# Performance work log

Hardware: AMD Instinct MI355X
Metric: run time of the kernel (lower is better)

## Reference

```python
import jax, jax.numpy as jnp
import numpy as np

# module hyperparameters (from init_kwargs)
K = 32          # out_channels / features per branch
THRESH = 20.0   # firing threshold
KWTA = 4        # winners per branch
RF = 512        # rf_size (number of branches)
L = 2048        # receptive-field length
T = 32          # timesteps (leading 'batch' dim in SpykeTorch)
C = 1           # in_channels


def setup_inputs() -> dict:
    key = jax.random.key(0)
    k1, k2, k3 = jax.random.split(key, 3)
    rec_field = jax.random.uniform(k1, (T, C, RF, L), dtype=jnp.float32)
    W = jax.random.normal(k2, (RF, K, C, L), dtype=jnp.float32)  # per-branch local-conv weights
    reward = jax.random.normal(k3, (1, 1, RF), dtype=jnp.float32)
    return {"rec_field": rec_field, "W": W, "reward": reward}


def _winner_mask(thr, spikes):
    """SpykeTorch sf.get_k_winners for a single branch with 1x1 spatial output.
    thr, spikes: (T, K) thresholded potentials and their sign (0/1).
    Returns a (K,) 0/1 mask over the kwta winning features.
    Score = earliest-spike-dominant total potential, exactly as in SpykeTorch:
      first  = T - sum_t spikes           (first spike time, clamped)
      values = thr[first, k]
      total  = sum_t (spikes*values + spikes * max(spikes*values)*T)
    With 1x1 spatial, inhibition_radius has no effect; picking then zeroing a
    feature == distinct top-k over features with a nonzero check.
    """
    first = jnp.clip((T - spikes.sum(0)).astype(jnp.int32), 0, T - 1)          # (K,)
    vals_at_first = jnp.take_along_axis(thr, first[None, :], axis=0)[0]        # (K,)
    trunc = spikes * vals_at_first[None, :]                                    # (T, K)
    v = trunc.max() * T
    total = (trunc + spikes * v).sum(0)                                        # (K,)
    top_vals, top_idx = jax.lax.top_k(total, KWTA)
    valid = (top_vals != 0).astype(thr.dtype)
    return jnp.zeros((K,), thr.dtype).at[top_idx].max(valid)


def reference(rec_field, W, reward):
    # per-branch local convolution: kernel covers the whole (1,L) input -> 1x1 output
    pot = jnp.einsum('tcrl,rkcl->rtk', rec_field, W)        # (RF, T, K)
    # sf.fire: keep potentials strictly above threshold (F.threshold semantics)
    thr = jnp.where(pot > THRESH, pot, jnp.zeros((), pot.dtype))
    spikes = jnp.sign(thr)
    # kWTA winner masks per branch (coefs), then masked sign
    mask = jax.vmap(_winner_mask)(thr, spikes)              # (RF, K)
    out = jnp.sign(thr * mask[:, None, :])                  # (RF, T, K)
    # torch: cat(dim=2) -> (T,K,RF,1) -> squeeze -> (T,K,RF) -> unsqueeze(1) -> (T,1,K,RF)
    return jnp.transpose(out, (1, 2, 0))[:, None, :, :]
```

## Files before the change

### kernel.cpp

```cpp
#include <hip/hip_runtime.h>
#include <cstdint>


typedef float vf4 __attribute__((ext_vector_type(4)));
typedef float vf2 __attribute__((ext_vector_type(2)));

#define RFN 512
#define TN  32
#define KN  32
#define LN  2048
#define CHUNK 128
#define NITER (LN / CHUNK)

__global__ __launch_bounds__(512, 4) void column1_fused(
    const float* __restrict__ rec,
    const float* __restrict__ wgt,
    float* __restrict__ out)
{
    __shared__ __align__(16) float lds[2 * 64 * CHUNK];
    __shared__ float thr_s[32 * 33];
    __shared__ float nspk_s[32], vals_s[32], cand_s[32], tot_s[32], mask_s[32];

    const int r    = blockIdx.x;
    const int tid  = threadIdx.x;
    const int lane = tid & 63;
    const int wv   = tid >> 6;
    const int tg   = lane >> 3;
    const int kg   = lane & 7;

    const int c4 = tid & 31;
    const int r0 = tid >> 5;
    const float* gsrc[4];
    int ldoff[4];
#pragma unroll
    for (int s = 0; s < 4; ++s) {
        const int row = r0 + 16 * s;
        const float* g;
        if (row < 32) g = rec + ((size_t)(row * RFN + r)) * LN + (c4 << 2);
        else          g = wgt + ((size_t)(r * KN + (row - 32))) * LN + (c4 << 2);
        gsrc[s]  = g;
        ldoff[s] = row * CHUNK + ((c4 ^ (row & 31)) << 2);
    }

    vf4 stage[4];
#pragma unroll
    for (int s = 0; s < 4; ++s)
        stage[s] = __builtin_nontemporal_load((const vf4*)gsrc[s]);

    float acc[4][4];
#pragma unroll
    for (int jt = 0; jt < 4; ++jt)
#pragma unroll
        for (int jk = 0; jk < 4; ++jk) acc[jt][jk] = 0.0f;

    for (int it = 0; it < NITER; ++it) {
        float* buf = lds + (it & 1) * (64 * CHUNK);
#pragma unroll
        for (int s = 0; s < 4; ++s) *(vf4*)(buf + ldoff[s]) = stage[s];
        __syncthreads();
        if (it + 1 < NITER) {
#pragma unroll
            for (int s = 0; s < 4; ++s) {
                gsrc[s] += CHUNK;
                stage[s] = __builtin_nontemporal_load((const vf4*)gsrc[s]);
            }
        }
        const float* rs  = buf;
        const float* wsh = buf + 32 * CHUNK;
#pragma unroll
        for (int q = 0; q < 4; ++q) {
            const int qg = (wv << 2) + q;
            vf4 a[4], b[4];
#pragma unroll
            for (int j = 0; j < 4; ++j) {
                const int row = tg + 8 * j;
                a[j] = *(const vf4*)(rs + row * CHUNK + ((qg ^ (row & 31)) << 2));
            }
#pragma unroll
            for (int j = 0; j < 4; ++j) {
                const int row = kg + 8 * j;
                b[j] = *(const vf4*)(wsh + row * CHUNK + ((qg ^ (row & 31)) << 2));
            }
#pragma unroll
            for (int jt = 0; jt < 4; ++jt)
#pragma unroll
                for (int jk = 0; jk < 4; ++jk) {
                    float v0 = fmaf(a[jt].x, b[jk].x, acc[jt][jk]);
                    v0 = fmaf(a[jt].y, b[jk].y, v0);
                    v0 = fmaf(a[jt].z, b[jk].z, v0);
                    acc[jt][jk] = fmaf(a[jt].w, b[jk].w, v0);
                }
        }
    }

    __syncthreads();

    float* red = lds;
#pragma unroll
    for (int jt = 0; jt < 4; ++jt)
#pragma unroll
        for (int jk = 0; jk < 4; ++jk)
            red[(wv << 10) + (tg + 8 * jt) * 32 + (kg + 8 * jk)] = acc[jt][jk];
    __syncthreads();

    const int o2 = tid << 1;
    float pv0 = 0.0f, pv1 = 0.0f;
#pragma unroll
    for (int s = 0; s < 8; ++s) {
        vf2 p = *(const vf2*)(red + (s << 10) + o2);
        pv0 += p.x; pv1 += p.y;
    }
    {
        const float th0 = (pv0 > 20.0f) ? pv0 : 0.0f;
        const float th1 = (pv1 > 20.0f) ? pv1 : 0.0f;
        thr_s[(o2 >> 5) * 33 + (o2 & 31)]             = th0;
        thr_s[((o2 + 1) >> 5) * 33 + ((o2 + 1) & 31)] = th1;
    }
    __syncthreads();

    if (tid < 32) {
        const int k = tid;
        int ns = 0;
        for (int t = 0; t < 32; ++t) ns += (thr_s[t * 33 + k] > 0.0f) ? 1 : 0;
        int first = 32 - ns; if (first > 31) first = 31;
        const float vf = thr_s[first * 33 + k];
        nspk_s[k] = (float)ns;
        vals_s[k] = vf;
        cand_s[k] = (ns > 0) ? vf : 0.0f;
        mask_s[k] = 0.0f;
    }
    __syncthreads();

    if (tid == 0) {
        float vm = 0.0f;
        for (int k = 0; k < 32; ++k) vm = fmaxf(vm, cand_s[k]);
        const float v = vm * 32.0f;
        for (int k = 0; k < 32; ++k) tot_s[k] = nspk_s[k] * (vals_s[k] + v);
        for (int sel = 0; sel < 4; ++sel) {
            int best = 0; float bv = -1.0f;
            for (int k = 0; k < 32; ++k) {
                const float tv = tot_s[k];
                if (tv > bv) { bv = tv; best = k; }
            }
            if (bv > 0.0f) mask_s[best] = 1.0f;
            tot_s[best] = -1.0f;
        }
    }
    __syncthreads();

#pragma unroll
    for (int e = 0; e < 2; ++e) {
        const int oo = o2 + e;
        const int t = oo >> 5, k = oo & 31;
        const float v = (thr_s[t * 33 + k] > 0.0f && mask_s[k] > 0.0f) ? 1.0f : 0.0f;
        __builtin_nontemporal_store(v, out + (size_t)t * (KN * RFN) + k * RFN + r);
    }
}

extern "C" void kernel_launch(void* const* d_in, const int* in_sizes, int n_in,
                              void* d_out, int out_size, void* d_ws, size_t ws_size,
                              hipStream_t stream) {
    const float* rec = (const float*)d_in[0];
    const float* wgt = (const float*)d_in[1];
    float* out = (float*)d_out;
    column1_fused<<<dim3(RFN), dim3(512), 0, stream>>>(rec, wgt, out);
}
```

Measured before the change: 279.7 us.

## Deepen global prefetch to two chunks ahead with custom LDS-only barrier

Splits the register staging into two sets so global loads are issued two chunks ahead of their use instead of one, keeping more memory traffic in flight. It also replaces __syncthreads with a barrier that waits only on LDS counters and not on outstanding global loads, so prefetches are no longer drained at each barrier. This costs extra VGPRs for the second staging set, which could lower occupancy under the 4-blocks launch bound.

```diff
diff --git a/kernel.cpp b/kernel.cpp
--- a/kernel.cpp
+++ b/kernel.cpp
@@ -11,6 +11,12 @@
 #define LN  2048
 #define CHUNK 128
 #define NITER (LN / CHUNK)
+
+#define BARW() do {                                         \
+    asm volatile("s_waitcnt lgkmcnt(0)" ::: "memory");      \
+    __builtin_amdgcn_s_barrier();                           \
+    __builtin_amdgcn_sched_barrier(0);                      \
+} while (0)
 
 __global__ __launch_bounds__(512, 4) void column1_fused(
     const float* __restrict__ rec,
@@ -30,7 +36,8 @@
 
     const int c4 = tid & 31;
     const int r0 = tid >> 5;
-    const float* gsrc[4];
+    const float* gA[4];
+    const float* gB[4];
     int ldoff[4];
 #pragma unroll
     for (int s = 0; s < 4; ++s) {
@@ -38,14 +45,22 @@
         const float* g;
         if (row < 32) g = rec + ((size_t)(row * RFN + r)) * LN + (c4 << 2);
         else          g = wgt + ((size_t)(r * KN + (row - 32))) * LN + (c4 << 2);
-        gsrc[s]  = g;
+        gA[s] = g;
+        gB[s] = g + CHUNK;
         ldoff[s] = row * CHUNK + ((c4 ^ (row & 31)) << 2);
     }
 
-    vf4 stage[4];
-#pragma unroll
-    for (int s = 0; s < 4; ++s)
-        stage[s] = __builtin_nontemporal_load((const vf4*)gsrc[s]);
+    vf4 sA[4], sB[4];
+#pragma unroll
+    for (int s = 0; s < 4; ++s) {
+        sA[s] = __builtin_nontemporal_load((const vf4*)gA[s]);
+        gA[s] += 2 * CHUNK;
+    }
+#pragma unroll
+    for (int s = 0; s < 4; ++s) {
+        sB[s] = __builtin_nontemporal_load((const vf4*)gB[s]);
+        gB[s] += 2 * CHUNK;
+    }
 
     float acc[4][4];
 #pragma unroll
@@ -53,18 +68,7 @@
 #pragma unroll
         for (int jk = 0; jk < 4; ++jk) acc[jt][jk] = 0.0f;
 
-    for (int it = 0; it < NITER; ++it) {
-        float* buf = lds + (it & 1) * (64 * CHUNK);
-#pragma unroll
-        for (int s = 0; s < 4; ++s) *(vf4*)(buf + ldoff[s]) = stage[s];
-        __syncthreads();
-        if (it + 1 < NITER) {
-#pragma unroll
-            for (int s = 0; s < 4; ++s) {
-                gsrc[s] += CHUNK;
-                stage[s] = __builtin_nontemporal_load((const vf4*)gsrc[s]);
-            }
-        }
+    auto compute = [&](const float* buf) {
         const float* rs  = buf;
         const float* wsh = buf + 32 * CHUNK;
 #pragma unroll
@@ -90,6 +94,37 @@
                     v0 = fmaf(a[jt].z, b[jk].z, v0);
                     acc[jt][jk] = fmaf(a[jt].w, b[jk].w, v0);
                 }
+        }
+    };
+
+    for (int it = 0; it < NITER; it += 2) {
+        {
+            float* buf = lds;
+#pragma unroll
+            for (int s = 0; s < 4; ++s) *(vf4*)(buf + ldoff[s]) = sA[s];
+            BARW();
+            if (it + 2 < NITER) {
+#pragma unroll
+                for (int s = 0; s < 4; ++s) {
+                    sA[s] = __builtin_nontemporal_load((const vf4*)gA[s]);
+                    gA[s] += 2 * CHUNK;
+                }
+            }
+            compute(buf);
+        }
+        {
+            float* buf = lds + 64 * CHUNK;
+#pragma unroll
+            for (int s = 0; s < 4; ++s) *(vf4*)(buf + ldoff[s]) = sB[s];
+            BARW();
+            if (it + 3 < NITER) {
+#pragma unroll
+                for (int s = 0; s < 4; ++s) {
+                    sB[s] = __builtin_nontemporal_load((const vf4*)gB[s]);
+                    gB[s] += 2 * CHUNK;
+                }
+            }
+            compute(buf);
         }
     }
 
```

After: 511.4 us. +82.8%, slower.
